# Kernel tuning notes

Measured on AMD Instinct MI355X. Metric: run time of the kernel, lower is better.

## Reference

```python
import jax, jax.numpy as jnp
import numpy as np

HIDDEN = 1024
N_EXPERTS = 8
CAP_FACTOR = 1.1
LN_EPS = 1e-5


def setup_inputs() -> dict:
    key = jax.random.key(0)
    ks = jax.random.split(key, 8)
    d, E, dff = HIDDEN, N_EXPERTS, 4 * HIDDEN
    x = jax.random.normal(ks[0], (4, 2048, d), dtype=jnp.float32)
    gate_w = jax.random.normal(ks[1], (d, E), dtype=jnp.float32) / np.sqrt(d)
    ln_g = jnp.ones((E, d), dtype=jnp.float32)
    ln_b = jnp.zeros((E, d), dtype=jnp.float32)
    w1 = jax.random.normal(ks[2], (E, d, dff), dtype=jnp.float32) / np.sqrt(d)
    b1 = jnp.zeros((E, dff), dtype=jnp.float32)
    w2 = jax.random.normal(ks[3], (E, dff, d), dtype=jnp.float32) / np.sqrt(dff)
    b2 = jnp.zeros((E, d), dtype=jnp.float32)
    return {"x": x, "gate_w": gate_w, "ln_g": ln_g, "ln_b": ln_b,
            "w1": w1, "b1": b1, "w2": w2, "b2": b2}


def reference(x, gate_w, ln_g, ln_b, w1, b1, w2, b2):
    B, S, d = x.shape
    E = gate_w.shape[1]
    N = B * S
    cap = int(N / E * CAP_FACTOR)  # expert capacity

    xt = x.reshape(N, d)
    # Router: top-1 expert per token (max-subtract before softmax is a no-op)
    logits = xt @ gate_w                               # [N, E]
    probs = jax.nn.softmax(logits, axis=-1)
    eidx = jnp.argmax(probs, axis=-1)                  # [N] int

    onehot = jax.nn.one_hot(eidx, E, dtype=jnp.int32)  # [N, E]
    counts = onehot.sum(axis=0).astype(jnp.float32)    # pre-drop counts [E]

    # Deterministic capacity: keep first `cap` tokens per expert, drop rest.
    # (torch code drops randomly via multinomial; structure is identical.)
    pos = jnp.cumsum(onehot, axis=0) - 1               # [N, E]
    pos_tok = jnp.take_along_axis(pos, eidx[:, None], axis=1)[:, 0]  # [N]
    keep = (pos_tok < cap).astype(x.dtype)             # [N]
    pos_c = jnp.minimum(pos_tok, cap - 1)              # clamp; dropped tokens write zeros

    # Dispatch into per-expert buffers [E, cap, d]
    buf = jnp.zeros((E, cap, d), dtype=x.dtype).at[eidx, pos_c].add(xt * keep[:, None])

    # Per-expert FFN: LayerNorm -> Linear -> GELU -> Linear
    mu = buf.mean(axis=-1, keepdims=True)
    var = jnp.mean((buf - mu) ** 2, axis=-1, keepdims=True)
    nb = (buf - mu) * jax.lax.rsqrt(var + LN_EPS)
    nb = nb * ln_g[:, None, :] + ln_b[:, None, :]
    h = jax.nn.gelu(jnp.einsum('ecd,edf->ecf', nb, w1) + b1[:, None, :], approximate=False)
    y = jnp.einsum('ecf,efd->ecd', h, w2) + b2[:, None, :]  # [E, cap, d]

    # Combine: dropped tokens get zeros (matches torch output init)
    out_tok = y[eidx, pos_c] * keep[:, None]           # [N, d]
    output = out_tok.reshape(B, S, d)

    # Load-balancing loss: 1 - cosine(counts, uniform) * 0.01
    tokens_per_expert = N / E
    uniform = jnp.full((E,), tokens_per_expert, dtype=jnp.float32)
    cos = jnp.dot(counts, uniform) / (jnp.linalg.norm(counts) * jnp.linalg.norm(uniform) + 1e-8)
    loss = 1.0 - cos * 0.01
    return output, loss
```

## Files before the change

### kernel.cpp

```cpp
#include <hip/hip_runtime.h>
#include <cstdint>
#include <cstddef>

#define NTOK 8192
#define D    1024
#define DFF  4096
#define NEXP 8
#define CAP  1126
#define MROWS 1280

typedef float f32x4  __attribute__((ext_vector_type(4)));
typedef float f32x16 __attribute__((ext_vector_type(16)));
typedef __bf16 bf16x8 __attribute__((ext_vector_type(8)));

__device__ inline unsigned short f2bf(float f) {
    unsigned u = __float_as_uint(f);
    u += 0x7fffu + ((u >> 16) & 1u);
    return (unsigned short)(u >> 16);
}

__device__ inline float gelu(float x) {
    float z  = 0.70710678118654752f * x;
    float az = fabsf(z);
    float t  = 1.0f / fmaf(0.3275911f, az, 1.0f);
    float p  = t * fmaf(t, fmaf(t, fmaf(t, fmaf(t, 1.061405429f, -1.453152027f),
                                        1.421413741f), -0.284496736f), 0.254829592f);
    float ee = __expf(-az * az);
    float er = fmaf(-p, ee, 1.0f);
    er = __builtin_copysignf(er, z);
    return 0.5f * x * (1.0f + er);
}

__device__ inline void gload16(const void* g, void* l) {
    __builtin_amdgcn_global_load_lds(
        (const __attribute__((address_space(1))) unsigned int*)g,
        (__attribute__((address_space(3))) unsigned int*)l,
        16, 0, 0);
}

__device__ void transpose_tile_dev(const float* __restrict__ W, unsigned short* __restrict__ WT,
                                   int K, int N, int tb, char* smem)
{
    int tiles_k = K >> 7, tiles_n = N >> 7;
    int per_e = tiles_k * tiles_n;
    int e = tb / per_e, rem = tb % per_e;
    int kb = rem % tiles_k, nb = rem / tiles_k;
    const float* We = W + (size_t)e * K * N + (size_t)(kb * 128) * N + nb * 128;
    unsigned short* Oe = WT + (size_t)e * K * N + (size_t)(nb * 128) * K + kb * 128;
    float* lds = (float*)smem;
    int t = threadIdx.x;
    #pragma unroll
    for (int p = 0; p < 2; ++p) {
        __syncthreads();
        #pragma unroll
        for (int j = 0; j < 8; ++j) {
            int idx = j * 256 + t;
            int r = idx >> 5, c4 = idx & 31;
            const float4 v = *(const float4*)(We + (size_t)(p * 64 + r) * N + c4 * 4);
            *(float4*)(lds + r * 128 + c4 * 4) = v;
        }
        __syncthreads();
        int c = t >> 1, half = t & 1;
        const float* col = lds + (half * 32) * 128 + c;
        unsigned short* orow = Oe + (size_t)c * K + p * 64 + half * 32;
        #pragma unroll
        for (int q = 0; q < 4; ++q) {
            uint4 o;
            o.x = f2bf(col[(q*8+0)*128]) | ((unsigned)f2bf(col[(q*8+1)*128]) << 16);
            o.y = f2bf(col[(q*8+2)*128]) | ((unsigned)f2bf(col[(q*8+3)*128]) << 16);
            o.z = f2bf(col[(q*8+4)*128]) | ((unsigned)f2bf(col[(q*8+5)*128]) << 16);
            o.w = f2bf(col[(q*8+6)*128]) | ((unsigned)f2bf(col[(q*8+7)*128]) << 16);
            *(uint4*)(orow + q * 8) = o;
        }
    }
}

__global__ __launch_bounds__(256) void transpose_kernel(
    const float* __restrict__ W, unsigned short* __restrict__ WT, int K, int N)
{
    __shared__ __align__(16) char smem[32768];
    transpose_tile_dev(W, WT, K, N, blockIdx.x, smem);
}

__global__ __launch_bounds__(256) void router_kernel(
    const float* __restrict__ x, const float* __restrict__ gw, int* __restrict__ eidx)
{
    int tok  = blockIdx.x * 4 + (threadIdx.x >> 6);
    int lane = threadIdx.x & 63;
    const float* xr = x + (size_t)tok * D;
    float a[8] = {0.f,0.f,0.f,0.f,0.f,0.f,0.f,0.f};
    #pragma unroll
    for (int it = 0; it < D / 64; ++it) {
        int d = lane + it * 64;
        float xv = xr[d];
        const float4 g0 = *(const float4*)(gw + (size_t)d * 8);
        const float4 g1 = *(const float4*)(gw + (size_t)d * 8 + 4);
        a[0] += xv * g0.x; a[1] += xv * g0.y; a[2] += xv * g0.z; a[3] += xv * g0.w;
        a[4] += xv * g1.x; a[5] += xv * g1.y; a[6] += xv * g1.z; a[7] += xv * g1.w;
    }
    #pragma unroll
    for (int off = 32; off > 0; off >>= 1)
        #pragma unroll
        for (int e = 0; e < 8; ++e) a[e] += __shfl_xor(a[e], off, 64);
    if (lane == 0) {
        int bi = 0; float bv = a[0];
        #pragma unroll
        for (int e = 1; e < 8; ++e) if (a[e] > bv) { bv = a[e]; bi = e; }
        eidx[tok] = bi;
    }
}

__global__ __launch_bounds__(1024) void scan_kernel(
    const int* __restrict__ eidx, int* __restrict__ slot_map,
    int* __restrict__ kept_cnt, float* __restrict__ loss_out,
    int* __restrict__ droplist, int* __restrict__ dropcnt)
{
    __shared__ int sc[8][1024];
    __shared__ int dcnt;
    int t = threadIdx.x;
    if (t == 0) dcnt = 0;
    int le[8];
    int c[8] = {0,0,0,0,0,0,0,0};
    #pragma unroll
    for (int i = 0; i < 8; ++i) { le[i] = eidx[t * 8 + i]; c[le[i]]++; }
    int v[8];
    #pragma unroll
    for (int e = 0; e < 8; ++e) { v[e] = c[e]; sc[e][t] = v[e]; }
    __syncthreads();
    for (int s = 1; s < 1024; s <<= 1) {
        int add[8] = {0,0,0,0,0,0,0,0};
        if (t >= s) {
            #pragma unroll
            for (int e = 0; e < 8; ++e) add[e] = sc[e][t - s];
        }
        __syncthreads();
        #pragma unroll
        for (int e = 0; e < 8; ++e) { v[e] += add[e]; sc[e][t] = v[e]; }
        __syncthreads();
    }
    int base[8];
    #pragma unroll
    for (int e = 0; e < 8; ++e) base[e] = v[e] - c[e];
    #pragma unroll
    for (int i = 0; i < 8; ++i) {
        int e = le[i]; int pos = base[e]++;
        if (pos < CAP) slot_map[e * CAP + pos] = t * 8 + i;
        else { int s = atomicAdd(&dcnt, 1); droplist[s] = t * 8 + i; }
    }
    __syncthreads();
    if (t == 0) *dropcnt = dcnt;
    if (t == 1023) {
        float dotv = 0.f, ss = 0.f;
        #pragma unroll
        for (int e = 0; e < 8; ++e) {
            float cf = (float)v[e];
            kept_cnt[e] = v[e] < CAP ? v[e] : CAP;
            dotv += cf * 1024.0f;
            ss   += cf * cf;
        }
        float denom = sqrtf(ss) * (1024.0f * sqrtf(8.0f)) + 1e-8f;
        loss_out[0] = 1.0f - 0.01f * (dotv / denom);
    }
}

__global__ __launch_bounds__(256) void zero_dropped(
    const int* __restrict__ droplist, const int* __restrict__ dropcnt,
    float4* __restrict__ out)
{
    int n = (*dropcnt) * 256;
    for (int idx = blockIdx.x * 256 + threadIdx.x; idx < n; idx += gridDim.x * 256)
        out[(size_t)droplist[idx >> 8] * 256 + (idx & 255)] = make_float4(0.f,0.f,0.f,0.f);
}

__global__ __launch_bounds__(256) void dispatch_ln(
    const float* __restrict__ x, const float* __restrict__ lng, const float* __restrict__ lnb,
    const int* __restrict__ slot_map, const int* __restrict__ kept_cnt,
    unsigned short* __restrict__ xbuf)
{
    int p = blockIdx.x, e = blockIdx.y, tid = threadIdx.x;
    ushort4* dst = (ushort4*)(xbuf + ((size_t)e * MROWS + p) * D) + tid;
    if (p >= kept_cnt[e]) { *dst = make_ushort4(0, 0, 0, 0); return; }
    int tok = slot_map[e * CAP + p];
    const float4 xv = *((const float4*)(x + (size_t)tok * D) + tid);
    float s  = xv.x + xv.y + xv.z + xv.w;
    float ss = xv.x * xv.x + xv.y * xv.y + xv.z * xv.z + xv.w * xv.w;
    #pragma unroll
    for (int off = 32; off > 0; off >>= 1) {
        s  += __shfl_xor(s,  off, 64);
        ss += __shfl_xor(ss, off, 64);
    }
    __shared__ float red[8];
    int lane = tid & 63, wv = tid >> 6;
    if (lane == 0) { red[wv] = s; red[4 + wv] = ss; }
    __syncthreads();
    s  = red[0] + red[1] + red[2] + red[3];
    ss = red[4] + red[5] + red[6] + red[7];
    float mu = s * (1.0f / D);
    float rs = rsqrtf(ss * (1.0f / D) - mu * mu + 1e-5f);
    const float4 gv = *((const float4*)(lng + (size_t)e * D) + tid);
    const float4 bv = *((const float4*)(lnb + (size_t)e * D) + tid);
    ushort4 o;
    o.x = f2bf((xv.x - mu) * rs * gv.x + bv.x);
    o.y = f2bf((xv.y - mu) * rs * gv.y + bv.y);
    o.z = f2bf((xv.z - mu) * rs * gv.z + bv.z);
    o.w = f2bf((xv.w - mu) * rs * gv.w + bv.w);
    *dst = o;
}

template<int K, int N, int MODE>
__global__ __launch_bounds__(512, 2) void gemm_kernel(
    const unsigned short* __restrict__ A,
    const unsigned short* __restrict__ BT,
    const float* __restrict__ bias,
    unsigned short* __restrict__ Hout,
    float* __restrict__ Yout,
    const int* __restrict__ slot_map,
    const int* __restrict__ kept_cnt)
{
    constexpr int MB = MROWS / 256;
    constexpr int NB = N / 256;
    constexpr int GB = NEXP * MB * NB;
    constexpr int T  = K / 64;
    __shared__ __align__(16) char smem[131072];

    const int obid = blockIdx.x;
    const int q8 = GB >> 3, r8 = GB & 7;
    const int xcd = obid & 7, ii = obid >> 3;
    const int swz = (xcd < r8 ? xcd * (q8 + 1) : r8 * (q8 + 1) + (xcd - r8) * q8) + ii;
    const int mb = swz % MB;
    const int t2 = swz / MB;
    const int nb = t2 % NB;
    const int e  = t2 / NB;

    const int tid  = threadIdx.x;
    const int lane = tid & 63;
    const int l31  = lane & 31, hi = lane >> 5;
    const int wave = tid >> 6;
    const int wr = wave >> 2, wc = wave & 3;
    const unsigned short* Ae = A + ((size_t)e * MROWS + (size_t)mb * 256) * K;
    const unsigned short* Be = BT + ((size_t)e * N + (size_t)nb * 256) * K;
    f32x16 acc[4][2] = {};

    auto stageAB = [&](int buf, int kk) {
        char* sA = smem + buf * 65536;
        char* sB = sA + 32768;
        #pragma unroll
        for (int q = 0; q < 4; ++q) {
            int cid = q * 512 + tid;
            int row = cid >> 3, pp = cid & 7;
            int cc  = pp ^ ((row >> 1) & 7);
            gload16(Ae + (size_t)row * K + kk * 64 + cc * 8, sA + cid * 16);
            gload16(Be + (size_t)row * K + kk * 64 + cc * 8, sB + cid * 16);
        }
    };
    auto ldA = [&](const char* sA, int mblk, int ks) -> bf16x8 {
        int row = wr * 128 + mblk * 32 + l31;
        int c0  = 2 * ks + hi;
        return *(const bf16x8*)(sA + row * 128 + ((c0 ^ ((row >> 1) & 7)) << 4));
    };
    auto ldB = [&](const char* sB, int nblk, int ks) -> bf16x8 {
        int row = wc * 64 + nblk * 32 + l31;
        int c0  = 2 * ks + hi;
        return *(const bf16x8*)(sB + row * 128 + ((c0 ^ ((row >> 1) & 7)) << 4));
    };

    stageAB(0, 0);
    stageAB(1, 1);
    asm volatile("s_waitcnt vmcnt(8)" ::: "memory");
    __builtin_amdgcn_s_barrier();

    for (int t = 0; t < T; ++t) {
        const char* sA = smem + (t & 1) * 65536;
        const char* sB = sA + 32768;
        bf16x8 af[4][2], bfv[2][2];
        #pragma unroll
        for (int m = 0; m < 4; ++m) { af[m][0] = ldA(sA, m, 0); af[m][1] = ldA(sA, m, 1); }
        #pragma unroll
        for (int n = 0; n < 2; ++n) { bfv[n][0] = ldB(sB, n, 0); bfv[n][1] = ldB(sB, n, 1); }
        asm volatile("s_waitcnt lgkmcnt(0)" ::: "memory");
        __builtin_amdgcn_sched_barrier(0);
        __builtin_amdgcn_s_setprio(1);
        #pragma unroll
        for (int ks = 0; ks < 2; ++ks)
            #pragma unroll
            for (int m = 0; m < 4; ++m)
                #pragma unroll
                for (int n = 0; n < 2; ++n)
                    acc[m][n] = __builtin_amdgcn_mfma_f32_32x32x16_bf16(
                        bfv[n][ks], af[m][ks], acc[m][n], 0, 0, 0);
        __builtin_amdgcn_s_setprio(0);
        __builtin_amdgcn_sched_barrier(0);
        #pragma unroll
        for (int m = 0; m < 4; ++m) { af[m][0] = ldA(sA, m, 2); af[m][1] = ldA(sA, m, 3); }
        #pragma unroll
        for (int n = 0; n < 2; ++n) { bfv[n][0] = ldB(sB, n, 2); bfv[n][1] = ldB(sB, n, 3); }
        asm volatile("s_waitcnt lgkmcnt(0)" ::: "memory");
        __builtin_amdgcn_sched_barrier(0);
        __builtin_amdgcn_s_barrier();
        if (t + 2 < T) stageAB(t & 1, t + 2);
        __builtin_amdgcn_sched_barrier(0);
        __builtin_amdgcn_s_setprio(1);
        #pragma unroll
        for (int ks = 0; ks < 2; ++ks)
            #pragma unroll
            for (int m = 0; m < 4; ++m)
                #pragma unroll
                for (int n = 0; n < 2; ++n)
                    acc[m][n] = __builtin_amdgcn_mfma_f32_32x32x16_bf16(
                        bfv[n][ks], af[m][ks], acc[m][n], 0, 0, 0);
        __builtin_amdgcn_s_setprio(0);
        if (t < T - 1) {
            if (t + 2 < T) asm volatile("s_waitcnt vmcnt(8)" ::: "memory");
            else           asm volatile("s_waitcnt vmcnt(0)" ::: "memory");
            __builtin_amdgcn_s_barrier();
        }
    }

    const int kept = (MODE == 1) ? kept_cnt[e] : 0;
    #pragma unroll
    for (int m = 0; m < 4; ++m) {
        const int row = mb * 256 + wr * 128 + m * 32 + l31;
        int tok = 0; bool live = true;
        if (MODE == 1) {
            live = row < kept;
            tok = live ? slot_map[e * CAP + row] : 0;
        }
        #pragma unroll
        for (int n = 0; n < 2; ++n) {
            #pragma unroll
            for (int q = 0; q < 4; ++q) {
                const int colb = nb * 256 + wc * 64 + n * 32 + q * 8 + hi * 4;
                const float4 bv = *(const float4*)(bias + (size_t)e * N + colb);
                float v0 = acc[m][n][4*q+0] + bv.x;
                float v1 = acc[m][n][4*q+1] + bv.y;
                float v2 = acc[m][n][4*q+2] + bv.z;
                float v3 = acc[m][n][4*q+3] + bv.w;
                if (MODE == 0) {
                    ushort4 o;
                    o.x = f2bf(gelu(v0)); o.y = f2bf(gelu(v1));
                    o.z = f2bf(gelu(v2)); o.w = f2bf(gelu(v3));
                    *(ushort4*)(Hout + ((size_t)e * MROWS + row) * N + colb) = o;
                } else if (live) {
                    *(float4*)(Yout + (size_t)tok * D + colb) = make_float4(v0, v1, v2, v3);
                }
            }
        }
    }
}

extern "C" void kernel_launch(void* const* d_in, const int* in_sizes, int n_in,
                              void* d_out, int out_size, void* d_ws, size_t ws_size,
                              hipStream_t stream)
{
    const float* x   = (const float*)d_in[0];
    const float* gw  = (const float*)d_in[1];
    const float* lng = (const float*)d_in[2];
    const float* lnb = (const float*)d_in[3];
    const float* w1  = (const float*)d_in[4];
    const float* b1  = (const float*)d_in[5];
    const float* w2  = (const float*)d_in[6];
    const float* b2  = (const float*)d_in[7];
    float* out = (float*)d_out;
    char* ws = (char*)d_ws;

    unsigned short* wT   = (unsigned short*)ws;
    unsigned short* xbuf = (unsigned short*)(ws + 67108864);
    unsigned short* hbuf = (unsigned short*)(ws + 88080384);
    int* eidx     = (int*)(ws + 171966464);
    int* slot_map = eidx + NTOK;
    int* kept     = slot_map + NEXP * CAP;
    int* dropcnt  = kept + NEXP;
    int* droplist = dropcnt + 8;

    constexpr int GB1 = NEXP * (MROWS / 256) * (DFF / 256);
    constexpr int GB2 = NEXP * (MROWS / 256) * (D / 256);
    constexpr int TB1 = NEXP * (D / 128) * (DFF / 128);
    constexpr int TB2 = NEXP * (DFF / 128) * (D / 128);

    router_kernel<<<NTOK / 4, 256, 0, stream>>>(x, gw, eidx);
    scan_kernel<<<1, 1024, 0, stream>>>(eidx, slot_map, kept,
                                        out + (size_t)NTOK * D, droplist, dropcnt);
    zero_dropped<<<64, 256, 0, stream>>>(droplist, dropcnt, (float4*)out);
    dispatch_ln<<<dim3(MROWS, NEXP), 256, 0, stream>>>(x, lng, lnb, slot_map, kept, xbuf);

    transpose_kernel<<<TB1, 256, 0, stream>>>(w1, wT, D, DFF);
    gemm_kernel<D, DFF, 0><<<GB1, 512, 0, stream>>>(
        xbuf, wT, b1, hbuf, nullptr, slot_map, kept);

    transpose_kernel<<<TB2, 256, 0, stream>>>(w2, wT, DFF, D);
    gemm_kernel<DFF, D, 1><<<GB2, 512, 0, stream>>>(
        hbuf, wT, b2, nullptr, out, slot_map, kept);
}
```

Measured before the change: 374.8 us.

## Shrink GEMM tiles to 256x128x32 with 4 waves and simpler double buffering

The expert GEMM kernel drops from a 256x256 tile with K-step 64 and 8 waves to a 256x128 tile with K-step 32 and 4 waves. Shared memory falls from 128KB to 48KB so three blocks can share a CU. Swizzled global and LDS offsets are now precomputed once per thread. The two-stage software pipeline with split LDS reads and fine waitcnt control becomes a simple stage-next/compute-current loop that waits on vmcnt(0) each iteration. This doubles the grid for better CU fill, but it lowers data reuse per tile and exposes more load latency per step.

```diff
diff --git a/kernel.cpp b/kernel.cpp
--- a/kernel.cpp
+++ b/kernel.cpp
@@ -208,7 +208,7 @@
 }
 
 template<int K, int N, int MODE>
-__global__ __launch_bounds__(512, 2) void gemm_kernel(
+__global__ __launch_bounds__(256, 3) void gemm_kernel(
     const unsigned short* __restrict__ A,
     const unsigned short* __restrict__ BT,
     const float* __restrict__ bias,
@@ -218,10 +218,10 @@
     const int* __restrict__ kept_cnt)
 {
     constexpr int MB = MROWS / 256;
-    constexpr int NB = N / 256;
+    constexpr int NB = N / 128;
     constexpr int GB = NEXP * MB * NB;
-    constexpr int T  = K / 64;
-    __shared__ __align__(16) char smem[131072];
+    constexpr int T  = K / 32;
+    __shared__ __align__(16) char smem[49152];
 
     const int obid = blockIdx.x;
     const int q8 = GB >> 3, r8 = GB & 7;
@@ -236,49 +236,63 @@
     const int lane = tid & 63;
     const int l31  = lane & 31, hi = lane >> 5;
     const int wave = tid >> 6;
-    const int wr = wave >> 2, wc = wave & 3;
+    const int wr = wave >> 1, wc = wave & 1;
     const unsigned short* Ae = A + ((size_t)e * MROWS + (size_t)mb * 256) * K;
-    const unsigned short* Be = BT + ((size_t)e * N + (size_t)nb * 256) * K;
+    const unsigned short* Be = BT + ((size_t)e * N + (size_t)nb * 128) * K;
+
+    int srcA[4], srcB[2];
+    #pragma unroll
+    for (int q = 0; q < 4; ++q) {
+        int cid = q * 256 + tid;
+        int row = cid >> 2, pp = cid & 3;
+        srcA[q] = row * K + (pp ^ ((row >> 1) & 3)) * 8;
+    }
+    #pragma unroll
+    for (int q = 0; q < 2; ++q) {
+        int cid = q * 256 + tid;
+        int row = cid >> 2, pp = cid & 3;
+        srcB[q] = row * K + (pp ^ ((row >> 1) & 3)) * 8;
+    }
+    int offA[4][2], offB[2][2];
+    #pragma unroll
+    for (int m = 0; m < 4; ++m)
+        #pragma unroll
+        for (int ks = 0; ks < 2; ++ks) {
+            int row = wr * 128 + m * 32 + l31;
+            offA[m][ks] = row * 64 + (((2 * ks + hi) ^ ((row >> 1) & 3)) << 4);
+        }
+    #pragma unroll
+    for (int n = 0; n < 2; ++n)
+        #pragma unroll
+        for (int ks = 0; ks < 2; ++ks) {
+            int row = wc * 64 + n * 32 + l31;
+            offB[n][ks] = 16384 + row * 64 + (((2 * ks + hi) ^ ((row >> 1) & 3)) << 4);
+        }
+
     f32x16 acc[4][2] = {};
 
-    auto stageAB = [&](int buf, int kk) {
-        char* sA = smem + buf * 65536;
-        char* sB = sA + 32768;
-        #pragma unroll
-        for (int q = 0; q < 4; ++q) {
-            int cid = q * 512 + tid;
-            int row = cid >> 3, pp = cid & 7;
-            int cc  = pp ^ ((row >> 1) & 7);
-            gload16(Ae + (size_t)row * K + kk * 64 + cc * 8, sA + cid * 16);
-            gload16(Be + (size_t)row * K + kk * 64 + cc * 8, sB + cid * 16);
-        }
+    auto stage = [&](int buf, int kk) {
+        char* sb = smem + buf * 24576;
+        #pragma unroll
+        for (int q = 0; q < 4; ++q)
+            gload16(Ae + srcA[q] + kk * 32, sb + (q * 256 + tid) * 16);
+        #pragma unroll
+        for (int q = 0; q < 2; ++q)
+            gload16(Be + srcB[q] + kk * 32, sb + 16384 + (q * 256 + tid) * 16);
     };
-    auto ldA = [&](const char* sA, int mblk, int ks) -> bf16x8 {
-        int row = wr * 128 + mblk * 32 + l31;
-        int c0  = 2 * ks + hi;
-        return *(const bf16x8*)(sA + row * 128 + ((c0 ^ ((row >> 1) & 7)) << 4));
-    };
-    auto ldB = [&](const char* sB, int nblk, int ks) -> bf16x8 {
-        int row = wc * 64 + nblk * 32 + l31;
-        int c0  = 2 * ks + hi;
-        return *(const bf16x8*)(sB + row * 128 + ((c0 ^ ((row >> 1) & 7)) << 4));
-    };
-
-    stageAB(0, 0);
-    stageAB(1, 1);
-    asm volatile("s_waitcnt vmcnt(8)" ::: "memory");
-    __builtin_amdgcn_s_barrier();
-
-    for (int t = 0; t < T; ++t) {
-        const char* sA = smem + (t & 1) * 65536;
-        const char* sB = sA + 32768;
-        bf16x8 af[4][2], bfv[2][2];
-        #pragma unroll
-        for (int m = 0; m < 4; ++m) { af[m][0] = ldA(sA, m, 0); af[m][1] = ldA(sA, m, 1); }
-        #pragma unroll
-        for (int n = 0; n < 2; ++n) { bfv[n][0] = ldB(sB, n, 0); bfv[n][1] = ldB(sB, n, 1); }
-        asm volatile("s_waitcnt lgkmcnt(0)" ::: "memory");
-        __builtin_amdgcn_sched_barrier(0);
+    auto compute = [&](int buf) {
+        const char* sb = smem + buf * 24576;
+        bf16x8 af[4][2], bf[2][2];
+        #pragma unroll
+        for (int m = 0; m < 4; ++m) {
+            af[m][0] = *(const bf16x8*)(sb + offA[m][0]);
+            af[m][1] = *(const bf16x8*)(sb + offA[m][1]);
+        }
+        #pragma unroll
+        for (int n = 0; n < 2; ++n) {
+            bf[n][0] = *(const bf16x8*)(sb + offB[n][0]);
+            bf[n][1] = *(const bf16x8*)(sb + offB[n][1]);
+        }
         __builtin_amdgcn_s_setprio(1);
         #pragma unroll
         for (int ks = 0; ks < 2; ++ks)
@@ -287,34 +301,22 @@
                 #pragma unroll
                 for (int n = 0; n < 2; ++n)
                     acc[m][n] = __builtin_amdgcn_mfma_f32_32x32x16_bf16(
-                        bfv[n][ks], af[m][ks], acc[m][n], 0, 0, 0);
+                        bf[n][ks], af[m][ks], acc[m][n], 0, 0, 0);
         __builtin_amdgcn_s_setprio(0);
-        __builtin_amdgcn_sched_barrier(0);
-        #pragma unroll
-        for (int m = 0; m < 4; ++m) { af[m][0] = ldA(sA, m, 2); af[m][1] = ldA(sA, m, 3); }
-        #pragma unroll
-        for (int n = 0; n < 2; ++n) { bfv[n][0] = ldB(sB, n, 2); bfv[n][1] = ldB(sB, n, 3); }
-        asm volatile("s_waitcnt lgkmcnt(0)" ::: "memory");
-        __builtin_amdgcn_sched_barrier(0);
-        __builtin_amdgcn_s_barrier();
-        if (t + 2 < T) stageAB(t & 1, t + 2);
-        __builtin_amdgcn_sched_barrier(0);
-        __builtin_amdgcn_s_setprio(1);
-        #pragma unroll
-        for (int ks = 0; ks < 2; ++ks)
-            #pragma unroll
-            for (int m = 0; m < 4; ++m)
-                #pragma unroll
-                for (int n = 0; n < 2; ++n)
-                    acc[m][n] = __builtin_amdgcn_mfma_f32_32x32x16_bf16(
-                        bfv[n][ks], af[m][ks], acc[m][n], 0, 0, 0);
-        __builtin_amdgcn_s_setprio(0);
-        if (t < T - 1) {
-            if (t + 2 < T) asm volatile("s_waitcnt vmcnt(8)" ::: "memory");
-            else           asm volatile("s_waitcnt vmcnt(0)" ::: "memory");
-            __builtin_amdgcn_s_barrier();
-        }
-    }
+    };
+
+    stage(0, 0);
+    asm volatile("s_waitcnt vmcnt(0)" ::: "memory");
+    __syncthreads();
+    int cur = 0;
+    for (int t = 0; t + 1 < T; ++t) {
+        stage(cur ^ 1, t + 1);
+        compute(cur);
+        asm volatile("s_waitcnt vmcnt(0)" ::: "memory");
+        __syncthreads();
+        cur ^= 1;
+    }
+    compute(cur);
 
     const int kept = (MODE == 1) ? kept_cnt[e] : 0;
     #pragma unroll
@@ -329,7 +331,7 @@
         for (int n = 0; n < 2; ++n) {
             #pragma unroll
             for (int q = 0; q < 4; ++q) {
-                const int colb = nb * 256 + wc * 64 + n * 32 + q * 8 + hi * 4;
+                const int colb = nb * 128 + wc * 64 + n * 32 + q * 8 + hi * 4;
                 const float4 bv = *(const float4*)(bias + (size_t)e * N + colb);
                 float v0 = acc[m][n][4*q+0] + bv.x;
                 float v1 = acc[m][n][4*q+1] + bv.y;
@@ -372,8 +374,8 @@
     int* dropcnt  = kept + NEXP;
     int* droplist = dropcnt + 8;
 
-    constexpr int GB1 = NEXP * (MROWS / 256) * (DFF / 256);
-    constexpr int GB2 = NEXP * (MROWS / 256) * (D / 256);
+    constexpr int GB1 = NEXP * (MROWS / 256) * (DFF / 128);
+    constexpr int GB2 = NEXP * (MROWS / 256) * (D / 128);
     constexpr int TB1 = NEXP * (D / 128) * (DFF / 128);
     constexpr int TB2 = NEXP * (DFF / 128) * (D / 128);
 
@@ -384,10 +386,10 @@
     dispatch_ln<<<dim3(MROWS, NEXP), 256, 0, stream>>>(x, lng, lnb, slot_map, kept, xbuf);
 
     transpose_kernel<<<TB1, 256, 0, stream>>>(w1, wT, D, DFF);
-    gemm_kernel<D, DFF, 0><<<GB1, 512, 0, stream>>>(
+    gemm_kernel<D, DFF, 0><<<GB1, 256, 0, stream>>>(
         xbuf, wT, b1, hbuf, nullptr, slot_map, kept);
 
     transpose_kernel<<<TB2, 256, 0, stream>>>(w2, wT, DFF, D);
-    gemm_kernel<DFF, D, 1><<<GB2, 512, 0, stream>>>(
+    gemm_kernel<DFF, D, 1><<<GB2, 256, 0, stream>>>(
         hbuf, wT, b2, nullptr, out, slot_map, kept);
 }
```

Result: slower. 1.339 ms (+257.3%).
